# Kernel tuning notes

Measured on AMD Instinct MI355X. Metric: run time of the kernel, lower is better.

The kernel has to match this reference:

```python
import jax, jax.numpy as jnp
import numpy as np

B, C, H, W = 4, 256, 64, 64
INTER = C // 2
BN_EPS = 1e-5


def setup_inputs() -> dict:
    key = jax.random.key(0)
    ks = jax.random.split(key, 12)
    s = 0.05
    return {
        "x": jax.random.normal(ks[0], (B, C, H, W), dtype=jnp.float32),
        "theta_w": jax.random.normal(ks[1], (INTER, C), dtype=jnp.float32) * s,
        "theta_b": jax.random.normal(ks[2], (INTER,), dtype=jnp.float32) * s,
        "phi_w": jax.random.normal(ks[3], (INTER, C), dtype=jnp.float32) * s,
        "phi_b": jax.random.normal(ks[4], (INTER,), dtype=jnp.float32) * s,
        "g_w": jax.random.normal(ks[5], (INTER, C), dtype=jnp.float32) * s,
        "g_b": jax.random.normal(ks[6], (INTER,), dtype=jnp.float32) * s,
        "W_w": jax.random.normal(ks[7], (C, INTER), dtype=jnp.float32) * s,
        "W_b": jax.random.normal(ks[8], (C,), dtype=jnp.float32) * s,
        "bn_gamma": jnp.ones((C,), dtype=jnp.float32),
        "bn_beta": jnp.zeros((C,), dtype=jnp.float32),
    }


def _conv1x1(x, w, b):
    # 1x1 conv == per-pixel GEMM: (B,C,H,W) x (O,C) -> (B,O,H,W)
    return jnp.einsum("bchw,oc->bohw", x, w) + b[None, :, None, None]


def reference(x, theta_w, theta_b, phi_w, phi_b, g_w, g_b, W_w, W_b, bn_gamma, bn_beta):
    b, c, h, w = x.shape
    hw = h * w
    theta = _conv1x1(x, theta_w, theta_b).reshape(b, -1, hw)  # (B, inter, HW) -> queries
    phi = _conv1x1(x, phi_w, phi_b).reshape(b, -1, hw)        # (B, inter, HW) -> keys
    g = _conv1x1(x, g_w, g_b).reshape(b, -1, hw)              # (B, inter, HW) -> values
    # f[n,m] = <theta[:,n], phi[:,m]> over all HW spatial positions
    f = jnp.einsum("bin,bim->bnm", theta, phi)                # (B, HW, HW)
    attn = jax.nn.softmax(f, axis=-1)
    y = jnp.einsum("bnm,bim->bin", attn, g)                   # (B, inter, HW)
    y = y.reshape(b, c // 2, h, w)
    wy = _conv1x1(y, W_w, W_b)                                # (B, C, H, W)
    # BatchNorm2d (training-mode batch statistics, per channel)
    mean = jnp.mean(wy, axis=(0, 2, 3), keepdims=True)
    var = jnp.var(wy, axis=(0, 2, 3), keepdims=True)
    wy_bn = bn_gamma[None, :, None, None] * (wy - mean) * jax.lax.rsqrt(var + BN_EPS) + bn_beta[None, :, None, None]
    return wy_bn + x
```

## Files before the change

### kernel.cpp

```cpp
#include <hip/hip_runtime.h>
#include <hip/hip_bf16.h>

#define HWN   4096
#define CIN   256
#define NINTER 128
#define NBATCH 4
#define BN_EPS 1e-5f
#define LOG2E 1.4426950408889634f
#define SMAX  64.0f

typedef __bf16 bf16_t;
typedef __bf16 bf16x8 __attribute__((ext_vector_type(8)));
typedef __bf16 bf16x4 __attribute__((ext_vector_type(4)));
typedef float  f32x4  __attribute__((ext_vector_type(4)));
typedef float  f32x16 __attribute__((ext_vector_type(16)));

__device__ __forceinline__ float fexp2(float x) {
  return __builtin_amdgcn_exp2f(x);
}

__device__ __forceinline__ void split_bf16(float v, bf16_t& h, bf16_t& l) {
  h = (bf16_t)v;
  l = (bf16_t)(v - (float)h);
}

__global__ __launch_bounds__(256) void convert_weights(
    const float* __restrict__ tw, const float* __restrict__ pw,
    const float* __restrict__ gw, const float* __restrict__ ww,
    bf16_t* __restrict__ out) {
  int i = blockIdx.x * 256 + threadIdx.x;
  float v;
  if (i < 32768)        v = tw[i];
  else if (i < 65536)   v = pw[i - 32768];
  else if (i < 98304)   v = gw[i - 65536];
  else                  v = ww[i - 98304];
  bf16_t h, l;
  split_bf16(v, h, l);
  out[i] = h;
  out[131072 + i] = l;
}

__global__ __launch_bounds__(256, 4) void qkv_kernel(
    const float* __restrict__ x, const bf16_t* __restrict__ wbf,
    const float* __restrict__ tb, const float* __restrict__ pb,
    const float* __restrict__ gb,
    bf16_t* __restrict__ Qh, bf16_t* __restrict__ Kh, bf16_t* __restrict__ V) {
  const int ntb  = blockIdx.x;
  const int b    = blockIdx.y;
  const int tid  = threadIdx.x;
  const int lane = tid & 63;
  const int wv   = tid >> 6;
  const int l31  = lane & 31;
  const int half = lane >> 5;

  __shared__ __align__(16) bf16_t smem[4608];
  bf16_t (*xTh)[72] = (bf16_t(*)[72])smem;
  bf16_t (*xTl)[72] = (bf16_t(*)[72])(smem + 2304);
  bf16_t (*Tr)[136] = (bf16_t(*)[136])smem;

  const bf16_t* Th = wbf;
  const bf16_t* Tl = wbf + 131072;
  const bf16_t* Ph = wbf + 32768;
  const bf16_t* Pl = wbf + 131072 + 32768;
  const bf16_t* Gh = wbf + 65536;
  const float*  xb = x + (size_t)b * CIN * HWN + ntb * 32;

  f32x16 aq, ak, av;
#pragma unroll
  for (int i = 0; i < 16; i++) { aq[i] = 0.f; ak[i] = 0.f; av[i] = 0.f; }

  for (int c0 = 0; c0 < 256; c0 += 64) {
    __syncthreads();
#pragma unroll
    for (int i = 0; i < 8; i++) {
      int idx = tid + i * 256;
      int cc = idx >> 5;
      int nn = idx & 31;
      float v = xb[(size_t)(c0 + cc) * HWN + nn];
      bf16_t h, l;
      split_bf16(v, h, l);
      xTh[nn][cc] = h;
      xTl[nn][cc] = l;
    }
    __syncthreads();
#pragma unroll
    for (int kk = 0; kk < 64; kk += 16) {
      size_t woff = (size_t)(32 * wv + l31) * 256 + c0 + kk + half * 8;
      bf16x8 th = *(const bf16x8*)(Th + woff);
      bf16x8 tl = *(const bf16x8*)(Tl + woff);
      bf16x8 ph = *(const bf16x8*)(Ph + woff);
      bf16x8 pl = *(const bf16x8*)(Pl + woff);
      bf16x8 gh = *(const bf16x8*)(Gh + woff);
      bf16x8 bh = *(const bf16x8*)(&xTh[l31][kk + half * 8]);
      bf16x8 bl = *(const bf16x8*)(&xTl[l31][kk + half * 8]);
      aq = __builtin_amdgcn_mfma_f32_32x32x16_bf16(th, bh, aq, 0, 0, 0);
      aq = __builtin_amdgcn_mfma_f32_32x32x16_bf16(th, bl, aq, 0, 0, 0);
      aq = __builtin_amdgcn_mfma_f32_32x32x16_bf16(tl, bh, aq, 0, 0, 0);
      ak = __builtin_amdgcn_mfma_f32_32x32x16_bf16(ph, bh, ak, 0, 0, 0);
      ak = __builtin_amdgcn_mfma_f32_32x32x16_bf16(ph, bl, ak, 0, 0, 0);
      ak = __builtin_amdgcn_mfma_f32_32x32x16_bf16(pl, bh, ak, 0, 0, 0);
      av = __builtin_amdgcn_mfma_f32_32x32x16_bf16(gh, bh, av, 0, 0, 0);
    }
  }

  const int trow = tid >> 3;
  const int tc16 = (tid & 7) * 16;
  bf16_t* qh = Qh + ((size_t)b * HWN + ntb * 32) * NINTER;
  bf16_t* kh = Kh + ((size_t)b * HWN + ntb * 32) * NINTER;

#pragma unroll
  for (int rnd = 0; rnd < 2; rnd++) {
    __syncthreads();
#pragma unroll
    for (int rg = 0; rg < 4; rg++) {
      int och0 = 32 * wv + 8 * rg + 4 * half;
#pragma unroll
      for (int j = 0; j < 4; j++) {
        float v = (rnd == 0) ? (aq[rg * 4 + j] + tb[och0 + j]) * LOG2E
                             : (ak[rg * 4 + j] + pb[och0 + j]);
        Tr[l31][och0 + j] = (bf16_t)v;
      }
    }
    __syncthreads();
    bf16_t* dst = (rnd == 0) ? qh : kh;
    bf16x8 v0 = *(const bf16x8*)(&Tr[trow][tc16]);
    bf16x8 v1 = *(const bf16x8*)(&Tr[trow][tc16 + 8]);
    *(bf16x8*)(dst + (size_t)trow * NINTER + tc16) = v0;
    *(bf16x8*)(dst + (size_t)trow * NINTER + tc16 + 8) = v1;
  }

  const int n = ntb * 32 + l31;
  bf16_t* vd = V + (size_t)b * NINTER * HWN;
#pragma unroll
  for (int r = 0; r < 16; r++) {
    int och = 32 * wv + (r & 3) + 8 * (r >> 2) + 4 * half;
    vd[(size_t)och * HWN + n] = (bf16_t)(av[r] + gb[och]);
  }
}

template<int NCv>
__global__ __launch_bounds__(512, 2) void attn_kernel(
    const bf16_t* __restrict__ Qh, const bf16_t* __restrict__ Kh,
    const bf16_t* __restrict__ V,
    float* __restrict__ Opart, float* __restrict__ Lp) {
  constexpr int CH = HWN / NCv;
  constexpr int NT = CH / 64;
  const int qt    = blockIdx.x;
  const int chunk = blockIdx.y;
  const int b     = blockIdx.z;
  const int tid   = threadIdx.x;
  const int lane  = tid & 63;
  const int wv    = tid >> 6;
  const int l15   = lane & 15;
  const int quad  = lane >> 4;
  const int kbase = chunk * CH;

  __shared__ __align__(16) bf16_t Klds[64][136];
  __shared__ __align__(16) bf16_t Vlds[144][72];
  __shared__ __align__(16) bf16_t Plds[8][32][72];

  const bf16_t* Qhb = Qh + (size_t)b * HWN * NINTER;
  const bf16_t* Khb = Kh + (size_t)b * HWN * NINTER;
  const bf16_t* Vb  = V + (size_t)b * NINTER * HWN;

  if (tid < 144) {
    int row = 128 + tid / 9;
    int c8 = (tid % 9) * 8;
    bf16x8 v;
#pragma unroll
    for (int j = 0; j < 8; j++) v[j] = (bf16_t)((row == 128) ? 1.0f : 0.0f);
    *(bf16x8*)(&Vlds[row][c8]) = v;
  }

  bf16x8 qf[2][4];
#pragma unroll
  for (int qs = 0; qs < 2; qs++) {
    const int qrow = qt * 256 + wv * 32 + qs * 16 + l15;
#pragma unroll
    for (int kc = 0; kc < 4; kc++)
      qf[qs][kc] = *(const bf16x8*)(Qhb + (size_t)qrow * NINTER + kc * 32 + quad * 8);
  }

  f32x4 o[2][8], ol[2];
#pragma unroll
  for (int qs = 0; qs < 2; qs++) {
#pragma unroll
    for (int dt = 0; dt < 8; dt++)
#pragma unroll
      for (int i = 0; i < 4; i++) o[qs][dt][i] = 0.f;
#pragma unroll
    for (int i = 0; i < 4; i++) ol[qs][i] = 0.f;
  }

  const int krow = tid >> 4;
  const int kc8  = (tid & 15) * 8;
  const int vrow = tid >> 3;
  const int vc8  = (tid & 7) * 8;
  const bf16_t* kgp = Khb + (size_t)(kbase + krow) * NINTER + kc8;
  const bf16_t* vgp = Vb + (size_t)vrow * HWN + kbase + vc8;

  uint4 ka = *(const uint4*)(kgp);
  uint4 kb = *(const uint4*)(kgp + (size_t)32 * NINTER);
  uint4 va = *(const uint4*)(vgp);
  uint4 vb = *(const uint4*)(vgp + (size_t)64 * HWN);

  for (int t = 0; t < NT; t++) {
    __syncthreads();
    *(uint4*)(&Klds[krow][kc8]) = ka;
    *(uint4*)(&Klds[krow + 32][kc8]) = kb;
    *(uint4*)(&Vlds[vrow][vc8]) = va;
    *(uint4*)(&Vlds[vrow + 64][vc8]) = vb;
    __syncthreads();

    if (t + 1 < NT) {
      const bf16_t* kn = kgp + (size_t)(t + 1) * 64 * NINTER;
      const bf16_t* vn = vgp + (t + 1) * 64;
      ka = *(const uint4*)(kn);
      kb = *(const uint4*)(kn + (size_t)32 * NINTER);
      va = *(const uint4*)(vn);
      vb = *(const uint4*)(vn + (size_t)64 * HWN);
    }

    f32x4 s[2][4];
#pragma unroll
    for (int qs = 0; qs < 2; qs++)
#pragma unroll
      for (int ks = 0; ks < 4; ks++)
#pragma unroll
        for (int i = 0; i < 4; i++) s[qs][ks][i] = 0.f;
#pragma unroll
    for (int ks = 0; ks < 4; ks++)
#pragma unroll
      for (int kc = 0; kc < 4; kc++) {
        bf16x8 kf = *(const bf16x8*)(&Klds[ks * 16 + l15][kc * 32 + quad * 8]);
        s[0][ks] = __builtin_amdgcn_mfma_f32_16x16x32_bf16(kf, qf[0][kc], s[0][ks], 0, 0, 0);
        s[1][ks] = __builtin_amdgcn_mfma_f32_16x16x32_bf16(kf, qf[1][kc], s[1][ks], 0, 0, 0);
      }

#pragma unroll
    for (int qs = 0; qs < 2; qs++)
#pragma unroll
      for (int ks = 0; ks < 4; ks++) {
        bf16x4 p4;
#pragma unroll
        for (int r = 0; r < 4; r++)
          p4[r] = (bf16_t)fexp2(s[qs][ks][r] - SMAX);
        *(bf16x4*)(&Plds[wv][qs * 16 + l15][ks * 16 + quad * 4]) = p4;
      }

#pragma unroll
    for (int kh = 0; kh < 2; kh++) {
      bf16x8 pf0 = *(const bf16x8*)(&Plds[wv][l15][kh * 32 + quad * 8]);
      bf16x8 pf1 = *(const bf16x8*)(&Plds[wv][16 + l15][kh * 32 + quad * 8]);
#pragma unroll
      for (int dt = 0; dt < 8; dt++) {
        bf16x8 vf = *(const bf16x8*)(&Vlds[dt * 16 + l15][kh * 32 + quad * 8]);
        o[0][dt] = __builtin_amdgcn_mfma_f32_16x16x32_bf16(pf0, vf, o[0][dt], 0, 0, 0);
        o[1][dt] = __builtin_amdgcn_mfma_f32_16x16x32_bf16(pf1, vf, o[1][dt], 0, 0, 0);
      }
      bf16x8 vfl = *(const bf16x8*)(&Vlds[128 + l15][kh * 32 + quad * 8]);
      ol[0] = __builtin_amdgcn_mfma_f32_16x16x32_bf16(pf0, vfl, ol[0], 0, 0, 0);
      ol[1] = __builtin_amdgcn_mfma_f32_16x16x32_bf16(pf1, vfl, ol[1], 0, 0, 0);
    }
  }

  float* Ob = Opart + ((size_t)(b * NCv + chunk) * HWN) * NINTER;
#pragma unroll
  for (int qs = 0; qs < 2; qs++)
#pragma unroll
    for (int r = 0; r < 4; r++) {
      int n = qt * 256 + wv * 32 + qs * 16 + quad * 4 + r;
#pragma unroll
      for (int dt = 0; dt < 8; dt++)
        Ob[(size_t)n * NINTER + dt * 16 + l15] = o[qs][dt][r];
      if (l15 == 0)
        Lp[(size_t)(b * NCv + chunk) * HWN + n] = ol[qs][r];
    }
}

template<int NCv>
__global__ __launch_bounds__(256, 4) void wconv_kernel(
    const bf16_t* __restrict__ Wbf, const float* __restrict__ Opart,
    const float* __restrict__ Lp, const float* __restrict__ Wb,
    bf16_t* __restrict__ WY) {
  const int ntb = blockIdx.x;
  const int b   = blockIdx.y;
  const int tid = threadIdx.x;
  const int lane = tid & 63;
  const int wv   = tid >> 6;
  const int l31  = lane & 31;
  const int half = lane >> 5;

  __shared__ __align__(16) bf16_t Ylds[32][136];
  __shared__ float Linv[32];

  if (tid < 32) {
    int n = ntb * 32 + tid;
    float ls = 0.f;
#pragma unroll
    for (int c = 0; c < NCv; c++) ls += Lp[(size_t)(b * NCv + c) * HWN + n];
    Linv[tid] = 1.f / ls;
  }

  const int nrow = tid >> 3;
  const int dgrp = tid & 7;
  float oacc[16];
#pragma unroll
  for (int j = 0; j < 16; j++) oacc[j] = 0.f;
#pragma unroll
  for (int c = 0; c < NCv; c++) {
    const float* Op = Opart +
        ((size_t)(b * NCv + c) * HWN + ntb * 32 + nrow) * NINTER + dgrp * 16;
#pragma unroll
    for (int q = 0; q < 4; q++) {
      f32x4 v = *(const f32x4*)(Op + q * 4);
#pragma unroll
      for (int j = 0; j < 4; j++) oacc[q * 4 + j] += v[j];
    }
  }
  __syncthreads();
  {
    float inv = Linv[nrow];
    bf16x8 y0, y1;
#pragma unroll
    for (int j = 0; j < 8; j++) {
      y0[j] = (bf16_t)(oacc[j] * inv);
      y1[j] = (bf16_t)(oacc[8 + j] * inv);
    }
    *(bf16x8*)(&Ylds[nrow][dgrp * 16]) = y0;
    *(bf16x8*)(&Ylds[nrow][dgrp * 16 + 8]) = y1;
  }
  __syncthreads();

  const bf16_t* Wh = Wbf + 98304;
  f32x16 acc[2];
#pragma unroll
  for (int c = 0; c < 2; c++)
#pragma unroll
    for (int i = 0; i < 16; i++) acc[c][i] = 0.f;

#pragma unroll
  for (int k0 = 0; k0 < 128; k0 += 16) {
    bf16x8 a0 = *(const bf16x8*)(Wh + (size_t)(wv * 64 + l31) * NINTER + k0 + half * 8);
    bf16x8 a1 = *(const bf16x8*)(Wh + (size_t)(wv * 64 + 32 + l31) * NINTER + k0 + half * 8);
    bf16x8 b0 = *(const bf16x8*)(&Ylds[l31][k0 + half * 8]);
    acc[0] = __builtin_amdgcn_mfma_f32_32x32x16_bf16(a0, b0, acc[0], 0, 0, 0);
    acc[1] = __builtin_amdgcn_mfma_f32_32x32x16_bf16(a1, b0, acc[1], 0, 0, 0);
  }

  bf16_t* dst = WY + (size_t)b * 256 * HWN + ntb * 32;
#pragma unroll
  for (int ct = 0; ct < 2; ct++)
#pragma unroll
    for (int r = 0; r < 16; r++) {
      int co = wv * 64 + ct * 32 + (r & 3) + 8 * (r >> 2) + 4 * half;
      dst[(size_t)co * HWN + l31] = (bf16_t)(acc[ct][r] + Wb[co]);
    }
}

__global__ __launch_bounds__(256) void stats_kernel(
    const bf16_t* __restrict__ WY, float* __restrict__ stats) {
  const int c = blockIdx.x;
  const int tid = threadIdx.x;
  float s = 0.f, s2 = 0.f;
  for (int b = 0; b < NBATCH; b++) {
    const bf16_t* p = WY + ((size_t)b * 256 + c) * HWN;
    for (int i = tid * 8; i < HWN; i += 2048) {
      bf16x8 v8 = *(const bf16x8*)(p + i);
#pragma unroll
      for (int j = 0; j < 8; j++) {
        float v = (float)v8[j];
        s += v;
        s2 += v * v;
      }
    }
  }
#pragma unroll
  for (int off = 1; off < 64; off <<= 1) {
    s += __shfl_xor(s, off);
    s2 += __shfl_xor(s2, off);
  }
  __shared__ float red[8];
  int wv = tid >> 6;
  if ((tid & 63) == 0) { red[wv] = s; red[4 + wv] = s2; }
  __syncthreads();
  if (tid == 0) {
    float S = red[0] + red[1] + red[2] + red[3];
    float S2 = red[4] + red[5] + red[6] + red[7];
    float mean = S * (1.f / 16384.f);
    float var = S2 * (1.f / 16384.f) - mean * mean;
    stats[c] = mean;
    stats[256 + c] = rsqrtf(var + BN_EPS);
  }
}

__global__ __launch_bounds__(256) void bn_kernel(
    const bf16_t* __restrict__ WY, const float* __restrict__ x,
    const float* __restrict__ stats, const float* __restrict__ gamma,
    const float* __restrict__ beta, float* __restrict__ out) {
  int idx = blockIdx.x * 256 + threadIdx.x;
  int e = idx * 4;
  int c = (e >> 12) & 255;
  bf16x4 w4 = *(const bf16x4*)(WY + e);
  float4 xv = *(const float4*)(x + e);
  float mean = stats[c];
  float g = gamma[c] * stats[256 + c];
  float bb = beta[c];
  float4 o;
  o.x = g * ((float)w4[0] - mean) + bb + xv.x;
  o.y = g * ((float)w4[1] - mean) + bb + xv.y;
  o.z = g * ((float)w4[2] - mean) + bb + xv.z;
  o.w = g * ((float)w4[3] - mean) + bb + xv.w;
  *(float4*)(out + e) = o;
}

extern "C" void kernel_launch(void* const* d_in, const int* in_sizes, int n_in,
                              void* d_out, int out_size, void* d_ws, size_t ws_size,
                              hipStream_t stream) {
  const float* x       = (const float*)d_in[0];
  const float* theta_b = (const float*)d_in[2];
  const float* phi_b   = (const float*)d_in[4];
  const float* g_b     = (const float*)d_in[6];
  const float* W_b     = (const float*)d_in[8];
  const float* bn_g    = (const float*)d_in[9];
  const float* bn_b    = (const float*)d_in[10];
  float* out = (float*)d_out;

  const size_t NEED8 = 12582912ull + 67108864ull + 8388608ull + 524288ull +
                       524288ull + 2048ull;
  const int nc = (ws_size >= NEED8) ? 8 : 4;
  const size_t opb = (size_t)nc * HWN * NINTER * NBATCH * 4;
  const size_t lpb = (size_t)nc * HWN * NBATCH * 4;

  char* ws = (char*)d_ws;
  bf16_t* Qh  = (bf16_t*)(ws);
  bf16_t* Kh  = (bf16_t*)(ws + 4194304);
  bf16_t* V   = (bf16_t*)(ws + 8388608);
  float*  OP  = (float*)(ws + 12582912);
  bf16_t* WY  = (bf16_t*)(ws + 12582912 + opb);
  float*  LP  = (float*)(ws + 12582912 + opb + 8388608);
  bf16_t* WBF = (bf16_t*)(ws + 12582912 + opb + 8388608 + lpb);
  float*  ST  = (float*)(ws + 12582912 + opb + 8388608 + lpb + 524288);

  convert_weights<<<512, 256, 0, stream>>>(
      (const float*)d_in[1], (const float*)d_in[3],
      (const float*)d_in[5], (const float*)d_in[7], WBF);
  qkv_kernel<<<dim3(128, NBATCH), 256, 0, stream>>>(
      x, WBF, theta_b, phi_b, g_b, Qh, Kh, V);
  if (nc == 8) {
    attn_kernel<8><<<dim3(16, 8, NBATCH), 512, 0, stream>>>(Qh, Kh, V, OP, LP);
    wconv_kernel<8><<<dim3(128, NBATCH), 256, 0, stream>>>(WBF, OP, LP, W_b, WY);
  } else {
    attn_kernel<4><<<dim3(16, 4, NBATCH), 512, 0, stream>>>(Qh, Kh, V, OP, LP);
    wconv_kernel<4><<<dim3(128, NBATCH), 256, 0, stream>>>(WBF, OP, LP, W_b, WY);
  }
  stats_kernel<<<256, 256, 0, stream>>>(WY, ST);
  bn_kernel<<<4096, 256, 0, stream>>>(WY, x, ST, bn_g, bn_b, out);
}
```

Before: 192.5 us.

## Fuse BN statistics into wconv epilogue via atomics, fix 4 key chunks

Measured after the change: 315.3 us. +63.8%, slower.

```diff
diff --git a/kernel.cpp b/kernel.cpp
--- a/kernel.cpp
+++ b/kernel.cpp
@@ -139,7 +139,7 @@
 }
 
 template<int NCv>
-__global__ __launch_bounds__(512, 2) void attn_kernel(
+__global__ __launch_bounds__(512, 1) void attn_kernel(
     const bf16_t* __restrict__ Qh, const bf16_t* __restrict__ Kh,
     const bf16_t* __restrict__ V,
     float* __restrict__ Opart, float* __restrict__ Lp) {
@@ -282,7 +282,7 @@
 __global__ __launch_bounds__(256, 4) void wconv_kernel(
     const bf16_t* __restrict__ Wbf, const float* __restrict__ Opart,
     const float* __restrict__ Lp, const float* __restrict__ Wb,
-    bf16_t* __restrict__ WY) {
+    bf16_t* __restrict__ WY, float* __restrict__ stats) {
   const int ntb = blockIdx.x;
   const int b   = blockIdx.y;
   const int tid = threadIdx.x;
@@ -354,44 +354,20 @@
 #pragma unroll
     for (int r = 0; r < 16; r++) {
       int co = wv * 64 + ct * 32 + (r & 3) + 8 * (r >> 2) + 4 * half;
-      dst[(size_t)co * HWN + l31] = (bf16_t)(acc[ct][r] + Wb[co]);
-    }
-}
-
-__global__ __launch_bounds__(256) void stats_kernel(
-    const bf16_t* __restrict__ WY, float* __restrict__ stats) {
-  const int c = blockIdx.x;
-  const int tid = threadIdx.x;
-  float s = 0.f, s2 = 0.f;
-  for (int b = 0; b < NBATCH; b++) {
-    const bf16_t* p = WY + ((size_t)b * 256 + c) * HWN;
-    for (int i = tid * 8; i < HWN; i += 2048) {
-      bf16x8 v8 = *(const bf16x8*)(p + i);
-#pragma unroll
-      for (int j = 0; j < 8; j++) {
-        float v = (float)v8[j];
-        s += v;
-        s2 += v * v;
-      }
-    }
-  }
-#pragma unroll
-  for (int off = 1; off < 64; off <<= 1) {
-    s += __shfl_xor(s, off);
-    s2 += __shfl_xor(s2, off);
-  }
-  __shared__ float red[8];
-  int wv = tid >> 6;
-  if ((tid & 63) == 0) { red[wv] = s; red[4 + wv] = s2; }
-  __syncthreads();
-  if (tid == 0) {
-    float S = red[0] + red[1] + red[2] + red[3];
-    float S2 = red[4] + red[5] + red[6] + red[7];
-    float mean = S * (1.f / 16384.f);
-    float var = S2 * (1.f / 16384.f) - mean * mean;
-    stats[c] = mean;
-    stats[256 + c] = rsqrtf(var + BN_EPS);
-  }
+      bf16_t wy = (bf16_t)(acc[ct][r] + Wb[co]);
+      dst[(size_t)co * HWN + l31] = wy;
+      float v = (float)wy;
+      float s = v, s2 = v * v;
+#pragma unroll
+      for (int off = 1; off < 32; off <<= 1) {
+        s  += __shfl_xor(s, off);
+        s2 += __shfl_xor(s2, off);
+      }
+      if (l31 == 0) {
+        atomicAdd(&stats[co], s);
+        atomicAdd(&stats[256 + co], s2);
+      }
+    }
 }
 
 __global__ __launch_bounds__(256) void bn_kernel(
@@ -403,8 +379,11 @@
   int c = (e >> 12) & 255;
   bf16x4 w4 = *(const bf16x4*)(WY + e);
   float4 xv = *(const float4*)(x + e);
-  float mean = stats[c];
-  float g = gamma[c] * stats[256 + c];
+  float S  = stats[c];
+  float S2 = stats[256 + c];
+  float mean = S * (1.f / 16384.f);
+  float var = S2 * (1.f / 16384.f) - mean * mean;
+  float g = gamma[c] * rsqrtf(var + BN_EPS);
   float bb = beta[c];
   float4 o;
   o.x = g * ((float)w4[0] - mean) + bb + xv.x;
@@ -426,11 +405,9 @@
   const float* bn_b    = (const float*)d_in[10];
   float* out = (float*)d_out;
 
-  const size_t NEED8 = 12582912ull + 67108864ull + 8388608ull + 524288ull +
-                       524288ull + 2048ull;
-  const int nc = (ws_size >= NEED8) ? 8 : 4;
-  const size_t opb = (size_t)nc * HWN * NINTER * NBATCH * 4;
-  const size_t lpb = (size_t)nc * HWN * NBATCH * 4;
+  constexpr int NC = 4;
+  const size_t opb = (size_t)NC * HWN * NINTER * NBATCH * 4;
+  const size_t lpb = (size_t)NC * HWN * NBATCH * 4;
 
   char* ws = (char*)d_ws;
   bf16_t* Qh  = (bf16_t*)(ws);
@@ -442,18 +419,15 @@
   bf16_t* WBF = (bf16_t*)(ws + 12582912 + opb + 8388608 + lpb);
   float*  ST  = (float*)(ws + 12582912 + opb + 8388608 + lpb + 524288);
 
+  hipMemsetAsync(ST, 0, 2048, stream);
   convert_weights<<<512, 256, 0, stream>>>(
       (const float*)d_in[1], (const float*)d_in[3],
       (const float*)d_in[5], (const float*)d_in[7], WBF);
   qkv_kernel<<<dim3(128, NBATCH), 256, 0, stream>>>(
       x, WBF, theta_b, phi_b, g_b, Qh, Kh, V);
-  if (nc == 8) {
-    attn_kernel<8><<<dim3(16, 8, NBATCH), 512, 0, stream>>>(Qh, Kh, V, OP, LP);
-    wconv_kernel<8><<<dim3(128, NBATCH), 256, 0, stream>>>(WBF, OP, LP, W_b, WY);
-  } else {
-    attn_kernel<4><<<dim3(16, 4, NBATCH), 512, 0, stream>>>(Qh, Kh, V, OP, LP);
-    wconv_kernel<4><<<dim3(128, NBATCH), 256, 0, stream>>>(WBF, OP, LP, W_b, WY);
-  }
-  stats_kernel<<<256, 256, 0, stream>>>(WY, ST);
+  attn_kernel<NC><<<dim3(16, NC, NBATCH), 512, 0, stream>>>(
+      Qh, Kh, V, OP, LP);
+  wconv_kernel<NC><<<dim3(128, NBATCH), 256, 0, stream>>>(
+      WBF, OP, LP, W_b, WY, ST);
   bn_kernel<<<4096, 256, 0, stream>>>(WY, x, ST, bn_g, bn_b, out);
 }
```
